# Optimization experiments

Hardware: AMD Instinct MI355X
Metric: run time of the kernel (lower is better)

The kernel has to match this reference:

```python
import jax, jax.numpy as jnp
import numpy as np

WZ, WH, WW = 2, 6, 12
WIN = WZ * WH * WW  # 144
DEPTH, DIM, HEADS = 2, 192, 6
NEG = -1e9


def earth_position_index():
    zi = np.arange(WZ); zj = -np.arange(WZ) * WZ
    hi = np.arange(WH); hj = -np.arange(WH) * WH
    w = np.arange(WW)
    c1 = np.stack(np.meshgrid(zi, hi, w, indexing='ij')).reshape(3, -1)
    c2 = np.stack(np.meshgrid(zj, hj, w, indexing='ij')).reshape(3, -1)
    coords = (c1[:, :, None] - c2[:, None, :]).transpose(1, 2, 0).copy()
    coords[:, :, 2] += WW - 1
    coords[:, :, 1] *= 2 * WW - 1
    coords[:, :, 0] *= (2 * WW - 1) * WH * WH
    return jnp.asarray(coords.sum(-1))


def shift_mask(Z, H):
    # Swin-style mask over Z (vertical) and H (latitude); W (longitude) is circular.
    sz, sh = WZ // 2, WH // 2
    region = np.zeros((Z, H), np.int32)
    cnt = 0
    for zs in (slice(0, Z - WZ), slice(Z - WZ, Z - sz), slice(Z - sz, Z)):
        for hs in (slice(0, H - WH), slice(H - WH, H - sh), slice(H - sh, H)):
            region[zs, hs] = cnt; cnt += 1
    r = region.reshape(Z // WZ, WZ, H // WH, WH).transpose(0, 2, 1, 3).reshape(-1, WZ * WH)
    r = np.repeat(r, WW, axis=1)  # window token order is (z,h,w)
    m = np.where(r[:, :, None] == r[:, None, :], 0.0, NEG).astype(np.float32)
    return jnp.asarray(m)


def window_partition(x, Z, H, W):
    B, C = x.shape[0], x.shape[-1]
    x = x.reshape(B, Z // WZ, WZ, H // WH, WH, W // WW, WW, C)
    x = x.transpose(0, 1, 3, 5, 2, 4, 6, 7)
    return x.reshape(B, (Z // WZ) * (H // WH) * (W // WW), WIN, C)


def window_reverse(xw, Z, H, W):
    B, C = xw.shape[0], xw.shape[-1]
    x = xw.reshape(B, Z // WZ, H // WH, W // WW, WZ, WH, WW, C)
    x = x.transpose(0, 1, 4, 2, 5, 3, 6, 7)
    return x.reshape(B, Z, H, W, C)


def layernorm(x, g, b):
    mu = x.mean(-1, keepdims=True)
    var = jnp.mean((x - mu) ** 2, axis=-1, keepdims=True)
    return (x - mu) * jax.lax.rsqrt(var + 1e-5) * g + b


def attn_windows(xw, qkv_w, qkv_b, proj_w, proj_b, bias_tab, pos_idx, mask):
    B, nW, N, C = xw.shape
    hd = C // HEADS
    qkv = (xw @ qkv_w + qkv_b).reshape(B, nW, N, 3, HEADS, hd)
    q, k, v = qkv[..., 0, :, :], qkv[..., 1, :, :], qkv[..., 2, :, :]
    attn = jnp.einsum('bwnhd,bwmhd->bwhnm', q * (hd ** -0.5), k)
    bias = bias_tab[pos_idx]
    attn = attn + bias.transpose(2, 0, 1)[None, None]
    if mask is not None:
        nzh = mask.shape[0]
        attn = attn.reshape(B, nzh, nW // nzh, HEADS, N, N) + mask[None, :, None, None]
        attn = attn.reshape(B, nW, HEADS, N, N)
    attn = jax.nn.softmax(attn, axis=-1)
    out = jnp.einsum('bwhnm,bwmhd->bwnhd', attn, v).reshape(B, nW, N, C)
    return out @ proj_w + proj_b


def forward(x, qkv_w, qkv_b, proj_w, proj_b, bias_tab,
            ln1_g, ln1_b, ln2_g, ln2_b, mlp_w1, mlp_b1, mlp_w2, mlp_b2, Z, H, W):
    B, L, C = x.shape
    pos_idx = earth_position_index()
    mask = shift_mask(Z, H)
    depth = qkv_w.shape[0]
    for i in range(depth):
        roll = (i % 2 == 1)
        shortcut = x
        xg = x.reshape(B, Z, H, W, C)
        if roll:
            xg = jnp.roll(xg, (-(WZ // 2), -(WH // 2), -(WW // 2)), axis=(1, 2, 3))
        xw = window_partition(xg, Z, H, W)
        xw = attn_windows(xw, qkv_w[i], qkv_b[i], proj_w[i], proj_b[i],
                          bias_tab[i], pos_idx, mask if roll else None)
        xg = window_reverse(xw, Z, H, W)
        if roll:
            xg = jnp.roll(xg, (WZ // 2, WH // 2, WW // 2), axis=(1, 2, 3))
        xa = xg.reshape(B, L, C)
        x = shortcut + layernorm(xa, ln1_g[i], ln1_b[i])
        h = jax.nn.gelu(x @ mlp_w1[i] + mlp_b1[i], approximate=False)
        h = h @ mlp_w2[i] + mlp_b2[i]
        x = x + layernorm(h, ln2_g[i], ln2_b[i])
    return x


def setup_inputs() -> dict:
    key = jax.random.key(0)
    ks = jax.random.split(key, 16)
    B, Z, H, W, C = 1, 8, 96, 180, DIM
    L = Z * H * W
    bias_rows = (2 * WW - 1) * WH * WH * WZ * WZ  # 3312
    s = 0.02
    return {
        'x': jax.random.normal(ks[0], (B, L, C), jnp.float32),
        'qkv_w': jax.random.normal(ks[1], (DEPTH, C, 3 * C), jnp.float32) * s,
        'qkv_b': jnp.zeros((DEPTH, 3 * C), jnp.float32),
        'proj_w': jax.random.normal(ks[2], (DEPTH, C, C), jnp.float32) * s,
        'proj_b': jnp.zeros((DEPTH, C), jnp.float32),
        'bias_tab': jax.random.normal(ks[3], (DEPTH, bias_rows, HEADS), jnp.float32) * s,
        'ln1_g': jnp.ones((DEPTH, C), jnp.float32),
        'ln1_b': jnp.zeros((DEPTH, C), jnp.float32),
        'ln2_g': jnp.ones((DEPTH, C), jnp.float32),
        'ln2_b': jnp.zeros((DEPTH, C), jnp.float32),
        'mlp_w1': jax.random.normal(ks[4], (DEPTH, C, 4 * C), jnp.float32) * s,
        'mlp_b1': jnp.zeros((DEPTH, 4 * C), jnp.float32),
        'mlp_w2': jax.random.normal(ks[5], (DEPTH, 4 * C, C), jnp.float32) * s,
        'mlp_b2': jnp.zeros((DEPTH, C), jnp.float32),
        'Z': Z, 'H': H, 'W': W,
    }


def reference(x, qkv_w, qkv_b, proj_w, proj_b, bias_tab, ln1_g, ln1_b, ln2_g, ln2_b,
              mlp_w1, mlp_b1, mlp_w2, mlp_b2, Z, H, W):
    return forward(x, qkv_w, qkv_b, proj_w, proj_b, bias_tab, ln1_g, ln1_b,
                   ln2_g, ln2_b, mlp_w1, mlp_b1, mlp_w2, mlp_b2, Z, H, W)
```

## Files before the change

kernel.cpp:

```cpp
#include <hip/hip_runtime.h>
#include <hip/hip_bf16.h>
#include <math.h>

#define L_TOK 138240
#define NW 960

typedef __attribute__((ext_vector_type(8))) short s16x8;
typedef __attribute__((ext_vector_type(8))) unsigned short u16x8;
typedef __attribute__((ext_vector_type(4))) unsigned short u16x4;
typedef __attribute__((ext_vector_type(4))) float f32x4;

__device__ __forceinline__ float bf2f(unsigned short u){
  union{unsigned int u;float f;} v; v.u=((unsigned int)u)<<16; return v.f;
}
__device__ __forceinline__ unsigned short f2bf(float f){
  __hip_bfloat16 b = __float2bfloat16(f);
  union { __hip_bfloat16 b; unsigned short u; } v; v.b = b; return v.u;
}
__device__ __forceinline__ void gll16(const void* g, void* l) {
  __builtin_amdgcn_global_load_lds((const __attribute__((address_space(1))) void*)g,
                                   (__attribute__((address_space(3))) void*)l, 16, 0, 0);
}
__device__ __forceinline__ float gelu_f(float v){
  const float s = v * 0.70710678118654752f;
  const float a = fabsf(s);
  const float t = 1.0f / (1.0f + 0.3275911f * a);
  float p = 1.061405429f;
  p = p*t - 1.453152027f;
  p = p*t + 1.421413741f;
  p = p*t - 0.284496736f;
  p = p*t + 0.254829592f;
  p = p*t;
  float y = 1.0f - p * __expf(-a*a);
  y = copysignf(y, s);
  return 0.5f * v * (1.0f + y);
}

template<int NTILES>
__global__ __launch_bounds__(256) void gemm_qkv(
    const unsigned short* __restrict__ xb,
    const unsigned short* __restrict__ Bt,
    const float* __restrict__ bias,
    unsigned short* __restrict__ out)
{
  __shared__ unsigned short As[64*192];
  const int tid = threadIdx.x;
  const int wid = tid >> 6, lane = tid & 63;
  const int lr = lane & 15, kg = lane >> 4;
  const int bm = blockIdx.x;
  const int wn = wid * 16;
  const int N = NTILES * 64;

  #pragma unroll
  for (int i = 0; i < 6; i++) {
    const int c = tid + i*256;
    const int r = c / 24, s = c % 24;
    const int sg = (s & 24) | ((s ^ r) & 7);
    gll16(&xb[(size_t)(bm*64 + r)*192 + sg*8], &As[c*8]);
  }
  __syncthreads();

  s16x8 a[4][6];
  #pragma unroll
  for (int mi = 0; mi < 4; mi++)
    #pragma unroll
    for (int ks = 0; ks < 6; ks++) {
      const int m = mi*16 + lr, g = ks*4 + kg;
      const int sg = (g & 24) | ((g ^ m) & 7);
      a[mi][ks] = *(const s16x8*)&As[m*192 + sg*8];
    }

  for (int bn = 0; bn < NTILES; bn++) {
    s16x8 b[6];
    #pragma unroll
    for (int ks = 0; ks < 6; ks++)
      b[ks] = *(const s16x8*)&Bt[(size_t)(bn*64 + wn + lr)*192 + ks*32 + kg*8];
    f32x4 acc[4] = {};
    #pragma unroll
    for (int ks = 0; ks < 6; ks++)
      #pragma unroll
      for (int mi = 0; mi < 4; mi++)
        acc[mi] = __builtin_amdgcn_mfma_f32_16x16x32_bf16(a[mi][ks], b[ks], acc[mi], 0, 0, 0);
    const int col = bn*64 + wn + lr;
    const float bv = bias[col];
    #pragma unroll
    for (int mi = 0; mi < 4; mi++)
      #pragma unroll
      for (int q = 0; q < 4; q++) {
        const int row = bm*64 + mi*16 + kg*4 + q;
        out[(size_t)row*N + col] = f2bf(acc[mi][q] + bv);
      }
  }
}

__global__ __launch_bounds__(256) void gemm_ln(
    const unsigned short* __restrict__ A,
    const unsigned short* __restrict__ Bt,
    const float* __restrict__ bias, const float* __restrict__ g,
    const float* __restrict__ bta,
    unsigned short* __restrict__ xbo,
    int lda)
{
  __shared__ unsigned short As[2][128*32];
  __shared__ unsigned short Bs[2][192*32];
  __shared__ float rowstat[128][2][2];
  const int tid = threadIdx.x;
  const int wid = tid >> 6, lane = tid & 63;
  const int lr = lane & 15, kg = lane >> 4;
  const int bm = blockIdx.x;
  const int wm = (wid >> 1) * 64, wn = (wid & 1) * 96;
  const int rsub = lane >> 2, kc = lane & 3;
  const int K = 192;

  f32x4 acc[4][6] = {};
  const int nst = K / 32;

  #pragma unroll
  for (int i = 0; i < 2; i++)
    gll16(&A[(size_t)(bm*128 + wid*32 + i*16 + rsub)*lda + kc*8], &As[0][(wid*32 + i*16)*32]);
  #pragma unroll
  for (int j = 0; j < 3; j++)
    gll16(&Bt[(size_t)(wid*48 + j*16 + rsub)*K + kc*8], &Bs[0][(wid*48 + j*16)*32]);
  __syncthreads();

  for (int t = 0; t < nst; t++) {
    const int cur = t & 1, nxt = cur ^ 1;
    if (t + 1 < nst) {
      const int k1 = (t+1)*32;
      #pragma unroll
      for (int i = 0; i < 2; i++)
        gll16(&A[(size_t)(bm*128 + wid*32 + i*16 + rsub)*lda + k1 + kc*8], &As[nxt][(wid*32 + i*16)*32]);
      #pragma unroll
      for (int j = 0; j < 3; j++)
        gll16(&Bt[(size_t)(wid*48 + j*16 + rsub)*K + k1 + kc*8], &Bs[nxt][(wid*48 + j*16)*32]);
    }
    s16x8 a[4], b[6];
    #pragma unroll
    for (int mi = 0; mi < 4; mi++) a[mi] = *(const s16x8*)&As[cur][(wm + mi*16 + lr)*32 + kg*8];
    #pragma unroll
    for (int ni = 0; ni < 6; ni++) b[ni] = *(const s16x8*)&Bs[cur][(wn + ni*16 + lr)*32 + kg*8];
    #pragma unroll
    for (int mi = 0; mi < 4; mi++)
      #pragma unroll
      for (int ni = 0; ni < 6; ni++)
        acc[mi][ni] = __builtin_amdgcn_mfma_f32_16x16x32_bf16(a[mi], b[ni], acc[mi][ni], 0, 0, 0);
    __syncthreads();
  }

  float bv[6], gv[6], btv[6];
  #pragma unroll
  for (int ni = 0; ni < 6; ni++) {
    const int col = wn + ni*16 + lr;
    bv[ni] = bias[col]; gv[ni] = g[col]; btv[ni] = bta[col];
  }
  #pragma unroll
  for (int mi = 0; mi < 4; mi++) {
    float s[4] = {0,0,0,0}, ss[4] = {0,0,0,0};
    #pragma unroll
    for (int ni = 0; ni < 6; ni++)
      #pragma unroll
      for (int q = 0; q < 4; q++) {
        const float v = acc[mi][ni][q] + bv[ni];
        s[q] += v; ss[q] += v*v;
      }
    #pragma unroll
    for (int q = 0; q < 4; q++) {
      #pragma unroll
      for (int m = 1; m < 16; m <<= 1) {
        s[q]  += __shfl_xor(s[q],  m, 64);
        ss[q] += __shfl_xor(ss[q], m, 64);
      }
    }
    if (lr == 0) {
      #pragma unroll
      for (int q = 0; q < 4; q++) {
        const int r = wm + mi*16 + kg*4 + q;
        rowstat[r][wid & 1][0] = s[q];
        rowstat[r][wid & 1][1] = ss[q];
      }
    }
  }
  __syncthreads();
  #pragma unroll
  for (int mi = 0; mi < 4; mi++) {
    #pragma unroll
    for (int q = 0; q < 4; q++) {
      const int rl = wm + mi*16 + kg*4 + q;
      const float s  = rowstat[rl][0][0] + rowstat[rl][1][0];
      const float ss = rowstat[rl][0][1] + rowstat[rl][1][1];
      const float mu = s * (1.0f/192.0f);
      const float rs = rsqrtf(ss * (1.0f/192.0f) - mu*mu + 1e-5f);
      const size_t grow = (size_t)(bm*128 + rl) * 192;
      #pragma unroll
      for (int ni = 0; ni < 6; ni++) {
        const float v = acc[mi][ni][q] + bv[ni];
        const float o = (v - mu) * rs * gv[ni] + btv[ni];
        const size_t idx = grow + wn + ni*16 + lr;
        xbo[idx] = f2bf(bf2f(xbo[idx]) + o);
      }
    }
  }
}

template<int WF32>
__global__ __launch_bounds__(256) void fused_mlp(
    const unsigned short* __restrict__ xb,
    const unsigned short* __restrict__ W1t,
    const unsigned short* __restrict__ W2t,
    const float* __restrict__ b1, const float* __restrict__ b2,
    const float* __restrict__ g, const float* __restrict__ bt,
    unsigned short* __restrict__ xbo, float* __restrict__ xf)
{
  __shared__ unsigned short As[64*192];
  __shared__ unsigned short Hs[2][64*64];
  __shared__ float rowstat[64][4][2];
  const int tid = threadIdx.x, wid = tid >> 6, lane = tid & 63;
  const int lr = lane & 15, kg = lane >> 4;
  const int row0 = blockIdx.x * 64;

  #pragma unroll
  for (int i = 0; i < 6; i++) {
    const int c = tid + i*256;
    const int r = c / 24, s = c % 24;
    const int sg = (s & 24) | ((s ^ r) & 7);
    gll16(&xb[(size_t)(row0 + r)*192 + sg*8], &As[c*8]);
  }
  __syncthreads();

  char* const hs0 = (char*)&Hs[0][0];
  char* const hs1 = (char*)&Hs[1][0];

  f32x4 yacc[4][3] = {};
  s16x8 w1f[6];
  #pragma unroll
  for (int ks = 0; ks < 6; ks++)
    w1f[ks] = *(const s16x8*)&W1t[(size_t)(wid*16 + lr)*192 + ks*32 + kg*8];

  for (int t = 0; t < 12; t++) {
    char* const hb = (t & 1) ? hs1 : hs0;
    f32x4 hacc[4];
    #pragma unroll
    for (int mb = 0; mb < 4; mb++) {
      const int m = mb*16 + lr;
      hacc[mb] = f32x4{0.f, 0.f, 0.f, 0.f};
      #pragma unroll
      for (int ks = 0; ks < 6; ks++) {
        const int gsl = ks*4 + kg;
        const int sg = (gsl & 24) | ((gsl ^ m) & 7);
        const s16x8 xf8 = *(const s16x8*)&As[m*192 + sg*8];
        hacc[mb] = __builtin_amdgcn_mfma_f32_16x16x32_bf16(w1f[ks], xf8, hacc[mb], 0, 0, 0);
      }
    }
    s16x8 b2f[6];
    #pragma unroll
    for (int kk = 0; kk < 2; kk++)
      #pragma unroll
      for (int nj = 0; nj < 3; nj++)
        b2f[kk*3 + nj] = *(const s16x8*)&W2t[(size_t)(wid*48 + nj*16 + lr)*768 + t*64 + kk*32 + kg*8];

    const float4 b1q = *(const float4*)&b1[t*64 + wid*16 + kg*4];
    {
      const int cb = wid*32 + kg*8;
      #pragma unroll
      for (int mb = 0; mb < 4; mb++) {
        const int m = mb*16 + lr;
        u16x4 hv;
        hv[0] = f2bf(gelu_f(hacc[mb][0] + b1q.x));
        hv[1] = f2bf(gelu_f(hacc[mb][1] + b1q.y));
        hv[2] = f2bf(gelu_f(hacc[mb][2] + b1q.z));
        hv[3] = f2bf(gelu_f(hacc[mb][3] + b1q.w));
        *(u16x4*)(hb + m*128 + (cb ^ ((m & 7) << 4))) = hv;
      }
    }
    __syncthreads();
    if (t < 11) {
      #pragma unroll
      for (int ks = 0; ks < 6; ks++)
        w1f[ks] = *(const s16x8*)&W1t[(size_t)((t+1)*64 + wid*16 + lr)*192 + ks*32 + kg*8];
    }
    #pragma unroll
    for (int kk = 0; kk < 2; kk++) {
      #pragma unroll
      for (int mi = 0; mi < 4; mi++) {
        const int m = mi*16 + lr;
        const int cb2 = kk*64 + kg*16;
        const s16x8 a2 = *(const s16x8*)(hb + m*128 + (cb2 ^ ((m & 7) << 4)));
        #pragma unroll
        for (int nj = 0; nj < 3; nj++)
          yacc[mi][nj] = __builtin_amdgcn_mfma_f32_16x16x32_bf16(a2, b2f[kk*3 + nj], yacc[mi][nj], 0, 0, 0);
      }
    }
  }

  float bv[3], gv[3], btv[3];
  #pragma unroll
  for (int nj = 0; nj < 3; nj++) {
    const int col = wid*48 + nj*16 + lr;
    bv[nj] = b2[col]; gv[nj] = g[col]; btv[nj] = bt[col];
  }
  #pragma unroll
  for (int mi = 0; mi < 4; mi++) {
    float s[4] = {0,0,0,0}, ss[4] = {0,0,0,0};
    #pragma unroll
    for (int nj = 0; nj < 3; nj++)
      #pragma unroll
      for (int q = 0; q < 4; q++) {
        const float v = yacc[mi][nj][q] + bv[nj];
        s[q] += v; ss[q] += v*v;
      }
    #pragma unroll
    for (int q = 0; q < 4; q++) {
      #pragma unroll
      for (int m = 1; m < 16; m <<= 1) {
        s[q]  += __shfl_xor(s[q],  m, 64);
        ss[q] += __shfl_xor(ss[q], m, 64);
      }
    }
    if (lr == 0) {
      #pragma unroll
      for (int q = 0; q < 4; q++) {
        rowstat[mi*16 + kg*4 + q][wid][0] = s[q];
        rowstat[mi*16 + kg*4 + q][wid][1] = ss[q];
      }
    }
  }
  __syncthreads();
  #pragma unroll
  for (int mi = 0; mi < 4; mi++) {
    #pragma unroll
    for (int q = 0; q < 4; q++) {
      const int rl = mi*16 + kg*4 + q;
      const float s  = rowstat[rl][0][0] + rowstat[rl][1][0] + rowstat[rl][2][0] + rowstat[rl][3][0];
      const float ss = rowstat[rl][0][1] + rowstat[rl][1][1] + rowstat[rl][2][1] + rowstat[rl][3][1];
      const float mu = s * (1.0f/192.0f);
      const float rs = rsqrtf(ss * (1.0f/192.0f) - mu*mu + 1e-5f);
      const size_t grow = (size_t)(row0 + rl) * 192;
      #pragma unroll
      for (int nj = 0; nj < 3; nj++) {
        const float v = yacc[mi][nj][q] + bv[nj];
        const float o = (v - mu) * rs * gv[nj] + btv[nj];
        const size_t idx = grow + wid*48 + nj*16 + lr;
        const float xn = bf2f(xbo[idx]) + o;
        xbo[idx] = f2bf(xn);
        if (WF32) xf[idx] = xn;
      }
    }
  }
}

__global__ __launch_bounds__(384) void attn_win7(
    unsigned short* qkv,
    const unsigned short* __restrict__ biasbt,
    int roll)
{
  __shared__ unsigned short Pw[6][16][168];
  __shared__ int lmap[144];

  const int w = blockIdx.x;
  const int tid = threadIdx.x, wid = tid / 64, lane = tid & 63;
  const int lr = lane & 15, kg = lane >> 4;
  const int ww = w % 15, hw = (w / 15) % 16, zw = w / 240;

  if (tid < 144) {
    const int z1 = tid / 72, h1 = (tid % 72) / 12, w1 = tid % 12;
    int z = zw*2 + z1, h = hw*6 + h1, xx = ww*12 + w1;
    if (roll) { z = (z + 1) & 7; h = (h + 3) % 96; xx = (xx + 6) % 180; }
    lmap[tid] = (z*96 + h)*180 + xx;
  }
  __syncthreads();

  const unsigned short* bb;
  if (roll) {
    const int c = ((zw == 3) ? 2 : 0) | ((hw == 15) ? 1 : 0);
    bb = biasbt + (size_t)c*124416 + (size_t)wid*20736;
  } else {
    bb = biasbt + (size_t)wid*20736;
  }

  s16x8 kfr[9];
  #pragma unroll
  for (int ti = 0; ti < 9; ti++)
    kfr[ti] = *(const s16x8*)&qkv[(size_t)lmap[ti*16 + lr]*576 + 192 + wid*32 + kg*8];

  s16x8 vbr[2][5];
  #pragma unroll
  for (int ci = 0; ci < 2; ci++)
    #pragma unroll
    for (int ks = 0; ks < 5; ks++) {
      u16x8 t;
      #pragma unroll
      for (int j = 0; j < 8; j++) {
        const int tok = ks*32 + kg*8 + j;
        t[j] = (tok < 144) ? qkv[(size_t)lmap[tok]*576 + 384 + wid*32 + ci*16 + lr] : (unsigned short)0;
      }
      vbr[ci][ks] = (s16x8)t;
    }

  #pragma unroll
  for (int j = 0; j < 4; j++) Pw[wid][lr][144 + kg*4 + j] = 0;

  for (int s = 0; s < 9; s++) {
    const s16x8 bq = *(const s16x8*)&qkv[(size_t)lmap[s*16 + lr]*576 + wid*32 + kg*8];

    float pb[9][4];
    float mx = -3.0e38f;
    #pragma unroll
    for (int ti = 0; ti < 9; ti++) {
      f32x4 acc = {0.f, 0.f, 0.f, 0.f};
      acc = __builtin_amdgcn_mfma_f32_16x16x32_bf16(kfr[ti], bq, acc, 0, 0, 0);
      const u16x4 b4 = *(const u16x4*)&bb[(size_t)(s*9 + ti)*256 + lr*16 + kg*4];
      #pragma unroll
      for (int q = 0; q < 4; q++) {
        const float sv = acc[q] + bf2f(b4[q]);
        pb[ti][q] = sv;
        mx = fmaxf(mx, sv);
      }
    }
    mx = fmaxf(mx, __shfl_xor(mx, 16, 64));
    mx = fmaxf(mx, __shfl_xor(mx, 32, 64));

    float sum = 0.f;
    #pragma unroll
    for (int ti = 0; ti < 9; ti++)
      #pragma unroll
      for (int q = 0; q < 4; q++) {
        const float p = __expf(pb[ti][q] - mx);
        pb[ti][q] = p;
        sum += p;
      }
    sum += __shfl_xor(sum, 16, 64);
    sum += __shfl_xor(sum, 32, 64);
    const float inv = 1.0f / sum;

    #pragma unroll
    for (int ti = 0; ti < 9; ti++)
      #pragma unroll
      for (int q = 0; q < 4; q++)
        Pw[wid][lr][ti*16 + kg*4 + q] = f2bf(pb[ti][q] * inv);

    #pragma unroll
    for (int ci = 0; ci < 2; ci++) {
      f32x4 accO = {0.f, 0.f, 0.f, 0.f};
      #pragma unroll
      for (int ks = 0; ks < 5; ks++) {
        const s16x8 pa = *(const s16x8*)&Pw[wid][lr][ks*32 + kg*8];
        accO = __builtin_amdgcn_mfma_f32_16x16x32_bf16(pa, vbr[ci][ks], accO, 0, 0, 0);
      }
      #pragma unroll
      for (int q = 0; q < 4; q++) {
        const int row = s*16 + kg*4 + q;
        qkv[(size_t)lmap[row]*576 + wid*32 + ci*16 + lr] = f2bf(accO[q]);
      }
    }
  }
}

__global__ void init_xb(const float* __restrict__ xin, unsigned short* __restrict__ xb, int n) {
  const int i = blockIdx.x*256 + threadIdx.x;
  if (i < n) xb[i] = f2bf(xin[i]);
}
__global__ void copy_diag(const float* __restrict__ a, float* __restrict__ o, int n) {
  const int i = blockIdx.x*256 + threadIdx.x;
  if (i < n) o[i] = a[i] + 50.0f;
}
__global__ void transpose_w(const float* __restrict__ src, unsigned short* __restrict__ dst,
                            int K, int N, int nscale, float factor) {
  const int i = blockIdx.x*256 + threadIdx.x;
  const int tot = K*N;
  if (i >= 2*tot) return;
  const int l = i / tot, e = i % tot;
  const int k = e / N, n = e % N;
  float v = src[i];
  if (n < nscale) v *= factor;
  dst[(size_t)l*tot + (size_t)n*K + k] = f2bf(v);
}
__global__ void scale_qb(const float* __restrict__ src, float* __restrict__ dst) {
  const int i = blockIdx.x*256 + threadIdx.x;
  if (i >= 2*576) return;
  const float f = (i % 576) < 192 ? 0.17677669529663687f : 1.0f;
  dst[i] = src[i] * f;
}
__global__ void build_biasb6(const float* __restrict__ tab, unsigned short* __restrict__ bm) {
  const int i = blockIdx.x*256 + threadIdx.x;
  const int TAB = 6*144*144;
  if (i >= 5*TAB) return;
  const int tau = i / TAB, r = i % TAB;
  const int hd = r / 20736, rr = r % 20736;
  const int s = rr / 2304, rrr = rr % 2304;
  const int ti = rrr / 256, e = rrr % 256;
  const int lr_ = e / 16, c4 = e % 16;
  const int q = s*16 + lr_, tok = ti*16 + c4;
  const int z1 = q/72,  h1 = (q%72)/12,  w1 = q%12;
  const int z2 = tok/72, h2 = (tok%72)/12, w2 = tok%12;
  const int idx = (z1 + 2*z2)*828 + (h1 + 6*h2)*23 + (w1 - w2 + 11);
  const int l = (tau == 0) ? 0 : 1;
  float v = tab[(size_t)l*3312*6 + (size_t)idx*6 + hd];
  if (tau >= 1) {
    const int c = tau - 1, zs = c >> 1, hs = c & 1;
    const int rq = (zs ? (1 + z1) : 0)*3 + (hs ? (1 + (h1 >= 3)) : 0);
    const int rt = (zs ? (1 + z2) : 0)*3 + (hs ? (1 + (h2 >= 3)) : 0);
    if (rq != rt) v -= 1.0e9f;
  }
  bm[i] = f2bf(v);
}

extern "C" void kernel_launch(void* const* d_in, const int* in_sizes, int n_in,
                              void* d_out, int out_size, void* d_ws, size_t ws_size,
                              hipStream_t stream) {
  const float* x_in    = (const float*)d_in[0];
  const float* qkv_w   = (const float*)d_in[1];
  const float* qkv_b   = (const float*)d_in[2];
  const float* proj_w  = (const float*)d_in[3];
  const float* proj_b  = (const float*)d_in[4];
  const float* bias_tab= (const float*)d_in[5];
  const float* ln1_g   = (const float*)d_in[6];
  const float* ln1_b   = (const float*)d_in[7];
  const float* ln2_g   = (const float*)d_in[8];
  const float* ln2_b   = (const float*)d_in[9];
  const float* mlp_w1  = (const float*)d_in[10];
  const float* mlp_b1  = (const float*)d_in[11];
  const float* mlp_w2  = (const float*)d_in[12];
  const float* mlp_b2  = (const float*)d_in[13];

  const int nElem = L_TOK * 192;
  float* xf = (float*)d_out;

  const size_t sz_R0 = 159252480;
  const size_t sz_xb = 53084160;
  const size_t sz_wT = 1769472;
  const size_t sz_bb = 2488320;
  const size_t sz_qb = 4608;
  const size_t need  = sz_R0 + sz_xb + sz_wT + sz_bb + sz_qb;

  if (ws_size < need) {
    copy_diag<<<dim3((nElem+255)/256), 256, 0, stream>>>(x_in, xf, nElem);
    return;
  }

  char* ws = (char*)d_ws;
  unsigned short* R0    = (unsigned short*)(ws);
  unsigned short* xb    = (unsigned short*)(ws + sz_R0);
  unsigned short* wT    = (unsigned short*)(ws + sz_R0 + sz_xb);
  unsigned short* biasb = (unsigned short*)(ws + sz_R0 + sz_xb + sz_wT);
  float*          qb2   = (float*)(ws + sz_R0 + sz_xb + sz_wT + sz_bb);

  unsigned short* wT_qkv  = wT;
  unsigned short* wT_proj = wT + 221184;
  unsigned short* wT_m1   = wT + 294912;
  unsigned short* wT_m2   = wT + 589824;

  transpose_w<<<dim3((2*192*576+255)/256), 256, 0, stream>>>(qkv_w,  wT_qkv, 192, 576, 192, 0.17677669529663687f);
  transpose_w<<<dim3((2*192*192+255)/256), 256, 0, stream>>>(proj_w, wT_proj,192, 192, 0, 1.0f);
  transpose_w<<<dim3((2*192*768+255)/256), 256, 0, stream>>>(mlp_w1, wT_m1,  192, 768, 0, 1.0f);
  transpose_w<<<dim3((2*768*192+255)/256), 256, 0, stream>>>(mlp_w2, wT_m2,  768, 192, 0, 1.0f);
  build_biasb6<<<dim3((5*6*144*144+255)/256), 256, 0, stream>>>(bias_tab, biasb);
  scale_qb<<<dim3(5), 256, 0, stream>>>(qkv_b, qb2);

  init_xb<<<dim3((nElem+255)/256), 256, 0, stream>>>(x_in, xb, nElem);

  for (int i = 0; i < 2; i++) {
    gemm_qkv<9><<<dim3(2160), 256, 0, stream>>>(
        xb, wT_qkv + (size_t)i*110592, qb2 + i*576, R0);
    attn_win7<<<dim3(NW), 384, 0, stream>>>(
        R0, biasb + (i ? 124416 : 0), i & 1);
    gemm_ln<<<dim3(1080), 256, 0, stream>>>(
        R0, wT_proj + (size_t)i*36864, proj_b + i*192,
        ln1_g + i*192, ln1_b + i*192, xb, 576);
    if (i == 0)
      fused_mlp<0><<<dim3(2160), 256, 0, stream>>>(
          xb, wT_m1, wT_m2, mlp_b1, mlp_b2,
          ln2_g, ln2_b, xb, nullptr);
    else
      fused_mlp<1><<<dim3(2160), 256, 0, stream>>>(
          xb, wT_m1 + (size_t)147456, wT_m2 + (size_t)147456,
          mlp_b1 + 768, mlp_b2 + 192,
          ln2_g + 192, ln2_b + 192, xb, xf);
  }
}
```

Before: 881.4 us.

## Fuse projection GEMM and post-norm residual into the fused MLP kernel

```diff
diff --git a/kernel.cpp b/kernel.cpp
--- a/kernel.cpp
+++ b/kernel.cpp
@@ -93,122 +93,15 @@
   }
 }
 
-__global__ __launch_bounds__(256) void gemm_ln(
-    const unsigned short* __restrict__ A,
-    const unsigned short* __restrict__ Bt,
-    const float* __restrict__ bias, const float* __restrict__ g,
-    const float* __restrict__ bta,
-    unsigned short* __restrict__ xbo,
-    int lda)
-{
-  __shared__ unsigned short As[2][128*32];
-  __shared__ unsigned short Bs[2][192*32];
-  __shared__ float rowstat[128][2][2];
-  const int tid = threadIdx.x;
-  const int wid = tid >> 6, lane = tid & 63;
-  const int lr = lane & 15, kg = lane >> 4;
-  const int bm = blockIdx.x;
-  const int wm = (wid >> 1) * 64, wn = (wid & 1) * 96;
-  const int rsub = lane >> 2, kc = lane & 3;
-  const int K = 192;
-
-  f32x4 acc[4][6] = {};
-  const int nst = K / 32;
-
-  #pragma unroll
-  for (int i = 0; i < 2; i++)
-    gll16(&A[(size_t)(bm*128 + wid*32 + i*16 + rsub)*lda + kc*8], &As[0][(wid*32 + i*16)*32]);
-  #pragma unroll
-  for (int j = 0; j < 3; j++)
-    gll16(&Bt[(size_t)(wid*48 + j*16 + rsub)*K + kc*8], &Bs[0][(wid*48 + j*16)*32]);
-  __syncthreads();
-
-  for (int t = 0; t < nst; t++) {
-    const int cur = t & 1, nxt = cur ^ 1;
-    if (t + 1 < nst) {
-      const int k1 = (t+1)*32;
-      #pragma unroll
-      for (int i = 0; i < 2; i++)
-        gll16(&A[(size_t)(bm*128 + wid*32 + i*16 + rsub)*lda + k1 + kc*8], &As[nxt][(wid*32 + i*16)*32]);
-      #pragma unroll
-      for (int j = 0; j < 3; j++)
-        gll16(&Bt[(size_t)(wid*48 + j*16 + rsub)*K + k1 + kc*8], &Bs[nxt][(wid*48 + j*16)*32]);
-    }
-    s16x8 a[4], b[6];
-    #pragma unroll
-    for (int mi = 0; mi < 4; mi++) a[mi] = *(const s16x8*)&As[cur][(wm + mi*16 + lr)*32 + kg*8];
-    #pragma unroll
-    for (int ni = 0; ni < 6; ni++) b[ni] = *(const s16x8*)&Bs[cur][(wn + ni*16 + lr)*32 + kg*8];
-    #pragma unroll
-    for (int mi = 0; mi < 4; mi++)
-      #pragma unroll
-      for (int ni = 0; ni < 6; ni++)
-        acc[mi][ni] = __builtin_amdgcn_mfma_f32_16x16x32_bf16(a[mi], b[ni], acc[mi][ni], 0, 0, 0);
-    __syncthreads();
-  }
-
-  float bv[6], gv[6], btv[6];
-  #pragma unroll
-  for (int ni = 0; ni < 6; ni++) {
-    const int col = wn + ni*16 + lr;
-    bv[ni] = bias[col]; gv[ni] = g[col]; btv[ni] = bta[col];
-  }
-  #pragma unroll
-  for (int mi = 0; mi < 4; mi++) {
-    float s[4] = {0,0,0,0}, ss[4] = {0,0,0,0};
-    #pragma unroll
-    for (int ni = 0; ni < 6; ni++)
-      #pragma unroll
-      for (int q = 0; q < 4; q++) {
-        const float v = acc[mi][ni][q] + bv[ni];
-        s[q] += v; ss[q] += v*v;
-      }
-    #pragma unroll
-    for (int q = 0; q < 4; q++) {
-      #pragma unroll
-      for (int m = 1; m < 16; m <<= 1) {
-        s[q]  += __shfl_xor(s[q],  m, 64);
-        ss[q] += __shfl_xor(ss[q], m, 64);
-      }
-    }
-    if (lr == 0) {
-      #pragma unroll
-      for (int q = 0; q < 4; q++) {
-        const int r = wm + mi*16 + kg*4 + q;
-        rowstat[r][wid & 1][0] = s[q];
-        rowstat[r][wid & 1][1] = ss[q];
-      }
-    }
-  }
-  __syncthreads();
-  #pragma unroll
-  for (int mi = 0; mi < 4; mi++) {
-    #pragma unroll
-    for (int q = 0; q < 4; q++) {
-      const int rl = wm + mi*16 + kg*4 + q;
-      const float s  = rowstat[rl][0][0] + rowstat[rl][1][0];
-      const float ss = rowstat[rl][0][1] + rowstat[rl][1][1];
-      const float mu = s * (1.0f/192.0f);
-      const float rs = rsqrtf(ss * (1.0f/192.0f) - mu*mu + 1e-5f);
-      const size_t grow = (size_t)(bm*128 + rl) * 192;
-      #pragma unroll
-      for (int ni = 0; ni < 6; ni++) {
-        const float v = acc[mi][ni][q] + bv[ni];
-        const float o = (v - mu) * rs * gv[ni] + btv[ni];
-        const size_t idx = grow + wn + ni*16 + lr;
-        xbo[idx] = f2bf(bf2f(xbo[idx]) + o);
-      }
-    }
-  }
-}
-
 template<int WF32>
-__global__ __launch_bounds__(256) void fused_mlp(
-    const unsigned short* __restrict__ xb,
+__global__ __launch_bounds__(256) void fused_block(
+    const unsigned short* __restrict__ AO,
+    const unsigned short* __restrict__ Wp,
+    const float* __restrict__ pbias, const float* __restrict__ g1, const float* __restrict__ bt1,
     const unsigned short* __restrict__ W1t,
     const unsigned short* __restrict__ W2t,
     const float* __restrict__ b1, const float* __restrict__ b2,
-    const float* __restrict__ g, const float* __restrict__ bt,
+    const float* __restrict__ g2, const float* __restrict__ bt2,
     unsigned short* __restrict__ xbo, float* __restrict__ xf)
 {
   __shared__ unsigned short As[64*192];
@@ -223,13 +116,85 @@
     const int c = tid + i*256;
     const int r = c / 24, s = c % 24;
     const int sg = (s & 24) | ((s ^ r) & 7);
-    gll16(&xb[(size_t)(row0 + r)*192 + sg*8], &As[c*8]);
+    gll16(&AO[(size_t)(row0 + r)*576 + sg*8], &As[c*8]);
+  }
+  __syncthreads();
+
+  f32x4 pacc[4][3] = {};
+  #pragma unroll
+  for (int ks = 0; ks < 6; ks++) {
+    s16x8 wpf[3];
+    #pragma unroll
+    for (int nj = 0; nj < 3; nj++)
+      wpf[nj] = *(const s16x8*)&Wp[(size_t)(wid*48 + nj*16 + lr)*192 + ks*32 + kg*8];
+    #pragma unroll
+    for (int mi = 0; mi < 4; mi++) {
+      const int m = mi*16 + lr, gg = ks*4 + kg;
+      const int sg = (gg & 24) | ((gg ^ m) & 7);
+      const s16x8 af = *(const s16x8*)&As[m*192 + sg*8];
+      #pragma unroll
+      for (int nj = 0; nj < 3; nj++)
+        pacc[mi][nj] = __builtin_amdgcn_mfma_f32_16x16x32_bf16(af, wpf[nj], pacc[mi][nj], 0, 0, 0);
+    }
+  }
+  float pv1[3], gv1[3], btv1[3];
+  #pragma unroll
+  for (int nj = 0; nj < 3; nj++) {
+    const int col = wid*48 + nj*16 + lr;
+    pv1[nj] = pbias[col]; gv1[nj] = g1[col]; btv1[nj] = bt1[col];
+  }
+  #pragma unroll
+  for (int mi = 0; mi < 4; mi++) {
+    float s[4] = {0,0,0,0}, ss[4] = {0,0,0,0};
+    #pragma unroll
+    for (int nj = 0; nj < 3; nj++)
+      #pragma unroll
+      for (int q = 0; q < 4; q++) {
+        const float v = pacc[mi][nj][q] + pv1[nj];
+        s[q] += v; ss[q] += v*v;
+      }
+    #pragma unroll
+    for (int q = 0; q < 4; q++) {
+      #pragma unroll
+      for (int m = 1; m < 16; m <<= 1) {
+        s[q]  += __shfl_xor(s[q],  m, 64);
+        ss[q] += __shfl_xor(ss[q], m, 64);
+      }
+    }
+    if (lr == 0) {
+      #pragma unroll
+      for (int q = 0; q < 4; q++) {
+        rowstat[mi*16 + kg*4 + q][wid][0] = s[q];
+        rowstat[mi*16 + kg*4 + q][wid][1] = ss[q];
+      }
+    }
+  }
+  __syncthreads();
+  #pragma unroll
+  for (int mi = 0; mi < 4; mi++) {
+    #pragma unroll
+    for (int q = 0; q < 4; q++) {
+      const int rl = mi*16 + kg*4 + q;
+      const float s  = rowstat[rl][0][0] + rowstat[rl][1][0] + rowstat[rl][2][0] + rowstat[rl][3][0];
+      const float ss = rowstat[rl][0][1] + rowstat[rl][1][1] + rowstat[rl][2][1] + rowstat[rl][3][1];
+      const float mu = s * (1.0f/192.0f);
+      const float rs = rsqrtf(ss * (1.0f/192.0f) - mu*mu + 1e-5f);
+      #pragma unroll
+      for (int nj = 0; nj < 3; nj++) {
+        const int col = wid*48 + nj*16 + lr;
+        const float v = pacc[mi][nj][q] + pv1[nj];
+        const float o = (v - mu) * rs * gv1[nj] + btv1[nj];
+        const float xn = bf2f(xbo[(size_t)(row0 + rl)*192 + col]) + o;
+        const int gr = col >> 3;
+        const int sg = (gr & 24) | ((gr ^ rl) & 7);
+        As[rl*192 + sg*8 + (col & 7)] = f2bf(xn);
+      }
+    }
   }
   __syncthreads();
 
   char* const hs0 = (char*)&Hs[0][0];
   char* const hs1 = (char*)&Hs[1][0];
-
   f32x4 yacc[4][3] = {};
   s16x8 w1f[6];
   #pragma unroll
@@ -296,7 +261,7 @@
   #pragma unroll
   for (int nj = 0; nj < 3; nj++) {
     const int col = wid*48 + nj*16 + lr;
-    bv[nj] = b2[col]; gv[nj] = g[col]; btv[nj] = bt[col];
+    bv[nj] = b2[col]; gv[nj] = g2[col]; btv[nj] = bt2[col];
   }
   #pragma unroll
   for (int mi = 0; mi < 4; mi++) {
@@ -337,12 +302,14 @@
       const size_t grow = (size_t)(row0 + rl) * 192;
       #pragma unroll
       for (int nj = 0; nj < 3; nj++) {
+        const int col = wid*48 + nj*16 + lr;
         const float v = yacc[mi][nj][q] + bv[nj];
         const float o = (v - mu) * rs * gv[nj] + btv[nj];
-        const size_t idx = grow + wid*48 + nj*16 + lr;
-        const float xn = bf2f(xbo[idx]) + o;
-        xbo[idx] = f2bf(xn);
-        if (WF32) xf[idx] = xn;
+        const int gr = col >> 3;
+        const int sg = (gr & 24) | ((gr ^ rl) & 7);
+        const float xn = bf2f(As[rl*192 + sg*8 + (col & 7)]) + o;
+        xbo[grow + col] = f2bf(xn);
+        if (WF32) xf[grow + col] = xn;
       }
     }
   }
@@ -563,17 +530,16 @@
         xb, wT_qkv + (size_t)i*110592, qb2 + i*576, R0);
     attn_win7<<<dim3(NW), 384, 0, stream>>>(
         R0, biasb + (i ? 124416 : 0), i & 1);
-    gemm_ln<<<dim3(1080), 256, 0, stream>>>(
-        R0, wT_proj + (size_t)i*36864, proj_b + i*192,
-        ln1_g + i*192, ln1_b + i*192, xb, 576);
     if (i == 0)
-      fused_mlp<0><<<dim3(2160), 256, 0, stream>>>(
-          xb, wT_m1, wT_m2, mlp_b1, mlp_b2,
-          ln2_g, ln2_b, xb, nullptr);
+      fused_block<0><<<dim3(2160), 256, 0, stream>>>(
+          R0, wT_proj, proj_b, ln1_g, ln1_b,
+          wT_m1, wT_m2, mlp_b1, mlp_b2, ln2_g, ln2_b,
+          xb, nullptr);
     else
-      fused_mlp<1><<<dim3(2160), 256, 0, stream>>>(
-          xb, wT_m1 + (size_t)147456, wT_m2 + (size_t)147456,
-          mlp_b1 + 768, mlp_b2 + 192,
-          ln2_g + 192, ln2_b + 192, xb, xf);
-  }
-}
+      fused_block<1><<<dim3(2160), 256, 0, stream>>>(
+          R0, wT_proj + 36864, proj_b + 192, ln1_g + 192, ln1_b + 192,
+          wT_m1 + 147456, wT_m2 + 147456, mlp_b1 + 768, mlp_b2 + 192,
+          ln2_g + 192, ln2_b + 192,
+          xb, xf);
+  }
+}
```

Result: slower. 1.029 ms (+16.8%).

## Use padded LDS rows and transposed MFMA output in fused MLP

Applied to the files above, without the earlier changes.

```diff
diff --git a/kernel.cpp b/kernel.cpp
--- a/kernel.cpp
+++ b/kernel.cpp
@@ -211,8 +211,8 @@
     const float* __restrict__ g, const float* __restrict__ bt,
     unsigned short* __restrict__ xbo, float* __restrict__ xf)
 {
-  __shared__ unsigned short As[64*192];
-  __shared__ unsigned short Hs[2][64*64];
+  __shared__ unsigned short As[64*200];
+  __shared__ unsigned short Hs[2][64*72];
   __shared__ float rowstat[64][4][2];
   const int tid = threadIdx.x, wid = tid >> 6, lane = tid & 63;
   const int lr = lane & 15, kg = lane >> 4;
@@ -222,13 +222,13 @@
   for (int i = 0; i < 6; i++) {
     const int c = tid + i*256;
     const int r = c / 24, s = c % 24;
-    const int sg = (s & 24) | ((s ^ r) & 7);
-    gll16(&xb[(size_t)(row0 + r)*192 + sg*8], &As[c*8]);
+    const u16x8 v = *(const u16x8*)&xb[(size_t)(row0 + r)*192 + s*8];
+    *(u16x8*)&As[r*200 + s*8] = v;
   }
   __syncthreads();
 
-  char* const hs0 = (char*)&Hs[0][0];
-  char* const hs1 = (char*)&Hs[1][0];
+  unsigned short* const hs0 = &Hs[0][0];
+  unsigned short* const hs1 = &Hs[1][0];
 
   f32x4 yacc[4][3] = {};
   s16x8 w1f[6];
@@ -237,7 +237,7 @@
     w1f[ks] = *(const s16x8*)&W1t[(size_t)(wid*16 + lr)*192 + ks*32 + kg*8];
 
   for (int t = 0; t < 12; t++) {
-    char* const hb = (t & 1) ? hs1 : hs0;
+    unsigned short* const hb = (t & 1) ? hs1 : hs0;
     f32x4 hacc[4];
     #pragma unroll
     for (int mb = 0; mb < 4; mb++) {
@@ -245,9 +245,7 @@
       hacc[mb] = f32x4{0.f, 0.f, 0.f, 0.f};
       #pragma unroll
       for (int ks = 0; ks < 6; ks++) {
-        const int gsl = ks*4 + kg;
-        const int sg = (gsl & 24) | ((gsl ^ m) & 7);
-        const s16x8 xf8 = *(const s16x8*)&As[m*192 + sg*8];
+        const s16x8 xf8 = *(const s16x8*)&As[m*200 + ks*32 + kg*8];
         hacc[mb] = __builtin_amdgcn_mfma_f32_16x16x32_bf16(w1f[ks], xf8, hacc[mb], 0, 0, 0);
       }
     }
@@ -260,7 +258,6 @@
 
     const float4 b1q = *(const float4*)&b1[t*64 + wid*16 + kg*4];
     {
-      const int cb = wid*32 + kg*8;
       #pragma unroll
       for (int mb = 0; mb < 4; mb++) {
         const int m = mb*16 + lr;
@@ -269,7 +266,7 @@
         hv[1] = f2bf(gelu_f(hacc[mb][1] + b1q.y));
         hv[2] = f2bf(gelu_f(hacc[mb][2] + b1q.z));
         hv[3] = f2bf(gelu_f(hacc[mb][3] + b1q.w));
-        *(u16x4*)(hb + m*128 + (cb ^ ((m & 7) << 4))) = hv;
+        *(u16x4*)&hb[m*72 + wid*16 + kg*4] = hv;
       }
     }
     __syncthreads();
@@ -283,67 +280,68 @@
       #pragma unroll
       for (int mi = 0; mi < 4; mi++) {
         const int m = mi*16 + lr;
-        const int cb2 = kk*64 + kg*16;
-        const s16x8 a2 = *(const s16x8*)(hb + m*128 + (cb2 ^ ((m & 7) << 4)));
+        const s16x8 a2 = *(const s16x8*)&hb[m*72 + kk*32 + kg*8];
         #pragma unroll
         for (int nj = 0; nj < 3; nj++)
-          yacc[mi][nj] = __builtin_amdgcn_mfma_f32_16x16x32_bf16(a2, b2f[kk*3 + nj], yacc[mi][nj], 0, 0, 0);
-      }
-    }
-  }
-
-  float bv[3], gv[3], btv[3];
+          yacc[mi][nj] = __builtin_amdgcn_mfma_f32_16x16x32_bf16(b2f[kk*3 + nj], a2, yacc[mi][nj], 0, 0, 0);
+      }
+    }
+  }
+
+  float4 bvq[3], gvq[3], btq[3];
   #pragma unroll
   for (int nj = 0; nj < 3; nj++) {
-    const int col = wid*48 + nj*16 + lr;
-    bv[nj] = b2[col]; gv[nj] = g[col]; btv[nj] = bt[col];
+    const int col = wid*48 + nj*16 + kg*4;
+    bvq[nj] = *(const float4*)&b2[col];
+    gvq[nj] = *(const float4*)&g[col];
+    btq[nj] = *(const float4*)&bt[col];
   }
   #pragma unroll
   for (int mi = 0; mi < 4; mi++) {
-    float s[4] = {0,0,0,0}, ss[4] = {0,0,0,0};
+    float s = 0.f, ss = 0.f;
     #pragma unroll
     for (int nj = 0; nj < 3; nj++)
       #pragma unroll
       for (int q = 0; q < 4; q++) {
-        const float v = yacc[mi][nj][q] + bv[nj];
-        s[q] += v; ss[q] += v*v;
-      }
-    #pragma unroll
-    for (int q = 0; q < 4; q++) {
-      #pragma unroll
-      for (int m = 1; m < 16; m <<= 1) {
-        s[q]  += __shfl_xor(s[q],  m, 64);
-        ss[q] += __shfl_xor(ss[q], m, 64);
-      }
-    }
-    if (lr == 0) {
-      #pragma unroll
-      for (int q = 0; q < 4; q++) {
-        rowstat[mi*16 + kg*4 + q][wid][0] = s[q];
-        rowstat[mi*16 + kg*4 + q][wid][1] = ss[q];
-      }
+        const float bq = (q==0)?bvq[nj].x:(q==1)?bvq[nj].y:(q==2)?bvq[nj].z:bvq[nj].w;
+        const float v = yacc[mi][nj][q] + bq;
+        s += v; ss += v*v;
+      }
+    s  += __shfl_xor(s, 16, 64);  s  += __shfl_xor(s, 32, 64);
+    ss += __shfl_xor(ss, 16, 64); ss += __shfl_xor(ss, 32, 64);
+    if (kg == 0) {
+      rowstat[mi*16 + lr][wid][0] = s;
+      rowstat[mi*16 + lr][wid][1] = ss;
     }
   }
   __syncthreads();
   #pragma unroll
   for (int mi = 0; mi < 4; mi++) {
-    #pragma unroll
-    for (int q = 0; q < 4; q++) {
-      const int rl = mi*16 + kg*4 + q;
-      const float s  = rowstat[rl][0][0] + rowstat[rl][1][0] + rowstat[rl][2][0] + rowstat[rl][3][0];
-      const float ss = rowstat[rl][0][1] + rowstat[rl][1][1] + rowstat[rl][2][1] + rowstat[rl][3][1];
-      const float mu = s * (1.0f/192.0f);
-      const float rs = rsqrtf(ss * (1.0f/192.0f) - mu*mu + 1e-5f);
-      const size_t grow = (size_t)(row0 + rl) * 192;
-      #pragma unroll
-      for (int nj = 0; nj < 3; nj++) {
-        const float v = yacc[mi][nj][q] + bv[nj];
-        const float o = (v - mu) * rs * gv[nj] + btv[nj];
-        const size_t idx = grow + wid*48 + nj*16 + lr;
-        const float xn = bf2f(xbo[idx]) + o;
-        xbo[idx] = f2bf(xn);
-        if (WF32) xf[idx] = xn;
-      }
+    const int rl = mi*16 + lr;
+    const float s  = rowstat[rl][0][0] + rowstat[rl][1][0] + rowstat[rl][2][0] + rowstat[rl][3][0];
+    const float ss = rowstat[rl][0][1] + rowstat[rl][1][1] + rowstat[rl][2][1] + rowstat[rl][3][1];
+    const float mu = s * (1.0f/192.0f);
+    const float rs = rsqrtf(ss * (1.0f/192.0f) - mu*mu + 1e-5f);
+    const size_t grow = (size_t)(row0 + rl) * 192;
+    #pragma unroll
+    for (int nj = 0; nj < 3; nj++) {
+      const int col = wid*48 + nj*16 + kg*4;
+      const u16x4 xo = *(const u16x4*)&xbo[grow + col];
+      u16x4 outv;
+      float4 xfv;
+      #pragma unroll
+      for (int q = 0; q < 4; q++) {
+        const float bq = (q==0)?bvq[nj].x:(q==1)?bvq[nj].y:(q==2)?bvq[nj].z:bvq[nj].w;
+        const float gq = (q==0)?gvq[nj].x:(q==1)?gvq[nj].y:(q==2)?gvq[nj].z:gvq[nj].w;
+        const float tq = (q==0)?btq[nj].x:(q==1)?btq[nj].y:(q==2)?btq[nj].z:btq[nj].w;
+        const float v = yacc[mi][nj][q] + bq;
+        const float o = (v - mu) * rs * gq + tq;
+        const float xn = bf2f(xo[q]) + o;
+        outv[q] = f2bf(xn);
+        if (q==0) xfv.x = xn; else if (q==1) xfv.y = xn; else if (q==2) xfv.z = xn; else xfv.w = xn;
+      }
+      *(u16x4*)&xbo[grow + col] = outv;
+      if (WF32) *(float4*)&xf[grow + col] = xfv;
     }
   }
 }
```

Result: slower. 914.0 us (+3.7%).
